# Optimization experiments

Hardware: AMD Instinct MI355X
Metric: run time of the kernel (lower is better)

The kernel has to match this reference:

```python
import jax, jax.numpy as jnp
import numpy as np
from jax import lax

EPS = 1e-5

def _layernorm(x, g, b):
    m = jnp.mean(x, axis=-1, keepdims=True)
    v = jnp.mean((x - m) ** 2, axis=-1, keepdims=True)
    return (x - m) * lax.rsqrt(v + EPS) * g + b

def _dwconv(x, H, W, w, b):
    # x: [B, N, C], w: [C, 1, 3, 3] (OIHW, depthwise), b: [C]
    B, N, C = x.shape
    xi = x.transpose(0, 2, 1).reshape(B, C, H, W)
    y = lax.conv_general_dilated(
        xi, w, window_strides=(1, 1), padding='SAME',
        feature_group_count=C,
        dimension_numbers=('NCHW', 'OIHW', 'NCHW'))
    y = y + b[None, :, None, None]
    return y.reshape(B, C, H * W).transpose(0, 2, 1)

def _channel_attn(x, groups, qkv_w, qkv_b, proj_w, proj_b):
    B, N, C = x.shape
    hd = C // groups
    qkv = x @ qkv_w.T + qkv_b                       # [B, N, 3C]
    qkv = qkv.reshape(B, N, 3, groups, hd)
    q, k, v = qkv[:, :, 0], qkv[:, :, 1], qkv[:, :, 2]   # [B, N, g, hd]
    q = q * (float(N) ** -0.5)
    attn = jnp.einsum('bngc,bngd->bgcd', q, k)      # [B, g, hd, hd]
    attn = jax.nn.softmax(attn, axis=-1)
    out = jnp.einsum('bgcd,bngd->bngc', attn, v)    # [B, N, g, hd]
    out = out.reshape(B, N, C)
    return out @ proj_w.T + proj_b

def _block(x, H, W, dw1_w, dw1_b, ln1_g, ln1_b, qkv_w, qkv_b, proj_w, proj_b,
           dw2_w, dw2_b, ln2_g, ln2_b, fc1_w, fc1_b, fc2_w, fc2_b, groups=8):
    # conv1 (no norm) + residual
    x = x + _dwconv(x, H, W, dw1_w, dw1_b)
    # prenorm channel attention + residual
    x = x + _channel_attn(_layernorm(x, ln1_g, ln1_b), groups, qkv_w, qkv_b, proj_w, proj_b)
    # conv2 (no norm) + residual
    x = x + _dwconv(x, H, W, dw2_w, dw2_b)
    # prenorm MLP + residual
    h = _layernorm(x, ln2_g, ln2_b)
    h = jax.nn.gelu(h @ fc1_w.T + fc1_b, approximate=False)
    x = x + (h @ fc2_w.T + fc2_b)
    return x

def setup_inputs() -> dict:
    key = jax.random.key(0)
    B, H, W, C, groups, ratio = 32, 32, 32, 768, 8, 4
    N, Ch = H * W, C * ratio
    ks = jax.random.split(key, 16)
    s = lambda fan: 1.0 / np.sqrt(fan)
    return {
        'x': jax.random.normal(ks[0], (B, N, C), jnp.float32),
        'H': H, 'W': W,
        'dw1_w': jax.random.normal(ks[1], (C, 1, 3, 3), jnp.float32) * s(9),
        'dw1_b': jnp.zeros((C,), jnp.float32),
        'ln1_g': jnp.ones((C,), jnp.float32),
        'ln1_b': jnp.zeros((C,), jnp.float32),
        'qkv_w': jax.random.normal(ks[2], (3 * C, C), jnp.float32) * s(C),
        'qkv_b': jnp.zeros((3 * C,), jnp.float32),
        'proj_w': jax.random.normal(ks[3], (C, C), jnp.float32) * s(C),
        'proj_b': jnp.zeros((C,), jnp.float32),
        'dw2_w': jax.random.normal(ks[4], (C, 1, 3, 3), jnp.float32) * s(9),
        'dw2_b': jnp.zeros((C,), jnp.float32),
        'ln2_g': jnp.ones((C,), jnp.float32),
        'ln2_b': jnp.zeros((C,), jnp.float32),
        'fc1_w': jax.random.normal(ks[5], (Ch, C), jnp.float32) * s(C),
        'fc1_b': jnp.zeros((Ch,), jnp.float32),
        'fc2_w': jax.random.normal(ks[6], (C, Ch), jnp.float32) * s(Ch),
        'fc2_b': jnp.zeros((C,), jnp.float32),
    }

def reference(x, H, W, dw1_w, dw1_b, ln1_g, ln1_b, qkv_w, qkv_b, proj_w, proj_b,
              dw2_w, dw2_b, ln2_g, ln2_b, fc1_w, fc1_b, fc2_w, fc2_b):
    return _block(x, H, W, dw1_w, dw1_b, ln1_g, ln1_b, qkv_w, qkv_b, proj_w, proj_b,
                  dw2_w, dw2_b, ln2_g, ln2_b, fc1_w, fc1_b, fc2_w, fc2_b)
```

## Files before the change

kernel.cpp:

```cpp
#include <hip/hip_runtime.h>

typedef unsigned short ushort_t;
typedef __bf16 v8bf __attribute__((ext_vector_type(8)));
typedef float v4f __attribute__((ext_vector_type(4)));

#define B_ 32
#define N_ 1024
#define C_ 768
#define G_ 8
#define HD_ 96
#define CH_ 3072
#define M_ 32768

static __device__ __forceinline__ float b2f(ushort_t u) {
    union { float f; unsigned int i; } z; z.i = ((unsigned int)u) << 16; return z.f;
}
static __device__ __forceinline__ ushort_t f2b(float f) {
    unsigned int u = __float_as_uint(f);
    u += 0x7fff + ((u >> 16) & 1);
    return (ushort_t)(u >> 16);
}
static __device__ __forceinline__ unsigned int pk2(float a, float b) {
    return (unsigned int)f2b(a) | ((unsigned int)f2b(b) << 16);
}

#define GLOAD_LDS16(g, l) __builtin_amdgcn_global_load_lds( \
    (const __attribute__((address_space(1))) unsigned int*)(g), \
    (__attribute__((address_space(3))) unsigned int*)(l), 16, 0, 0)

__global__ __launch_bounds__(256) void cvt_all(
    const float* __restrict__ a, const float* __restrict__ b,
    const float* __restrict__ c, const float* __restrict__ d,
    ushort_t* __restrict__ o)
{
    int blk = blockIdx.x;
    const float* src; ushort_t* dst; int off;
    if (blk < 1728)      { src = a; dst = o;                          off = blk; }
    else if (blk < 2304) { src = b; dst = o + 2304 * 768;             off = blk - 1728; }
    else if (blk < 4608) { src = c; dst = o + 2304 * 768 + 768 * 768; off = blk - 2304; }
    else                 { src = d; dst = o + 2304 * 768 + 768 * 768 + 3072 * 768; off = blk - 4608; }
    int i = (off * 256 + threadIdx.x) * 4;
    float4 v = *(const float4*)(src + i);
    uint2 p; p.x = pk2(v.x, v.y); p.y = pk2(v.z, v.w);
    *(uint2*)(dst + i) = p;
}

__global__ __launch_bounds__(256) void transpose_w2(
    const float* __restrict__ w1, const float* __restrict__ w2,
    float* __restrict__ wt1, float* __restrict__ wt2)
{
    int blk = blockIdx.x;
    const float* w = (blk < 27) ? w1 : w2;
    float* wt = (blk < 27) ? wt1 : wt2;
    int i = (blk % 27) * 256 + threadIdx.x;
    int c = i / 9, k = i % 9;
    wt[k * C_ + c] = w[i];
}

__global__ __launch_bounds__(256) void dwconv_add(
    const float* __restrict__ xin, const float* __restrict__ wt,
    const float* __restrict__ bias, float* __restrict__ out)
{
    int t = threadIdx.x;
    int bid = blockIdx.x;
    int cblk = bid % 6;
    int bhp = bid / 6;
    int b = bhp >> 4, hp = bhp & 15;
    int h0 = hp * 2;
    int tw = t >> 5;
    int c0 = cblk * 128 + (t & 31) * 4;
    int w0 = tw * 4;

    float4 tap[4][6];
#pragma unroll
    for (int dh = 0; dh < 4; dh++) {
        int hh = h0 + dh - 1;
        bool hok = (hh >= 0) && (hh < 32);
#pragma unroll
        for (int dw = 0; dw < 6; dw++) {
            int ww = w0 + dw - 1;
            bool ok = hok && (ww >= 0) && (ww < 32);
            if (ok)
                tap[dh][dw] = *(const float4*)(
                    xin + (size_t)((b << 10) | (hh << 5) | ww) * C_ + c0);
            else
                tap[dh][dw] = make_float4(0.f, 0.f, 0.f, 0.f);
        }
    }
    float4 wv[9];
#pragma unroll
    for (int k = 0; k < 9; k++)
        wv[k] = *(const float4*)(wt + k * C_ + c0);
    float4 bv = *(const float4*)(bias + c0);

#pragma unroll
    for (int row = 0; row < 2; row++) {
#pragma unroll
        for (int i = 0; i < 4; i++) {
            float4 acc = bv;
#pragma unroll
            for (int dh = 0; dh < 3; dh++)
#pragma unroll
                for (int dw = 0; dw < 3; dw++) {
                    float4 xv = tap[row + dh][i + dw];
                    float4 wk = wv[dh * 3 + dw];
                    acc.x += wk.x * xv.x; acc.y += wk.y * xv.y;
                    acc.z += wk.z * xv.z; acc.w += wk.w * xv.w;
                }
            float4 xr = tap[row + 1][i + 1];
            acc.x += xr.x; acc.y += xr.y; acc.z += xr.z; acc.w += xr.w;
            *(float4*)(out + (size_t)((b << 10) | ((h0 + row) << 5) | (w0 + i)) * C_ + c0) = acc;
        }
    }
}

__global__ __launch_bounds__(256) void layernorm_bf(
    const float* __restrict__ xin, const float* __restrict__ g,
    const float* __restrict__ bb, ushort_t* __restrict__ out)
{
    int row = blockIdx.x;
    int t = threadIdx.x;
    const float* xr = xin + (size_t)row * C_;
    float x0 = xr[t], x1 = xr[t + 256], x2 = xr[t + 512];
    float s1 = x0 + x1 + x2;
    float s2 = x0 * x0 + x1 * x1 + x2 * x2;
#pragma unroll
    for (int o = 32; o > 0; o >>= 1) {
        s1 += __shfl_xor(s1, o);
        s2 += __shfl_xor(s2, o);
    }
    __shared__ float red[8];
    if ((t & 63) == 0) { red[(t >> 6) * 2] = s1; red[(t >> 6) * 2 + 1] = s2; }
    __syncthreads();
    s1 = red[0] + red[2] + red[4] + red[6];
    s2 = red[1] + red[3] + red[5] + red[7];
    float m = s1 * (1.0f / 768.0f);
    float var = s2 * (1.0f / 768.0f) - m * m;
    float inv = rsqrtf(var + 1e-5f);
    ushort_t* orow = out + (size_t)row * C_;
    orow[t]       = f2b((x0 - m) * inv * g[t]       + bb[t]);
    orow[t + 256] = f2b((x1 - m) * inv * g[t + 256] + bb[t + 256]);
    orow[t + 512] = f2b((x2 - m) * inv * g[t + 512] + bb[t + 512]);
}

template <int EPI>
__global__ __launch_bounds__(256) void gemm_bt(
    const ushort_t* __restrict__ A, const ushort_t* __restrict__ W,
    const float* __restrict__ bias, const float* __restrict__ resid,
    void* __restrict__ outv, int M, int Nf, int K)
{
    __shared__ __align__(16) ushort_t ring[3][2][128 * 32];
    int t = threadIdx.x;
    int bm = blockIdx.x;
    int bn = blockIdx.y;
    int wave = t >> 6, lane = t & 63;
    int wm = (wave >> 1) * 64;
    int wn = (wave & 1) * 64;
    int row16 = lane & 15;
    int quad = lane >> 4;
    int qswz = (quad * 8) ^ (((row16 >> 1) & 3) * 8);

    int r0 = wave * 16 + (lane >> 2);
    int r1 = (wave + 4) * 16 + (lane >> 2);
    int c8s = ((lane & 3) ^ ((lane >> 3) & 3)) * 8;
    const ushort_t* Ag0 = A + (size_t)(bm * 128 + r0) * K + c8s;
    const ushort_t* Ag1 = A + (size_t)(bm * 128 + r1) * K + c8s;
    const ushort_t* Wg0 = W + (size_t)(bn * 128 + r0) * K + c8s;
    const ushort_t* Wg1 = W + (size_t)(bn * 128 + r1) * K + c8s;

    v4f acc[4][4];
#pragma unroll
    for (int i = 0; i < 4; i++)
#pragma unroll
        for (int j = 0; j < 4; j++) acc[i][j] = (v4f){0.f, 0.f, 0.f, 0.f};

    const int NT = K >> 5;

    auto STAGE = [&](int kt) {
        int s = kt % 3;
        ushort_t* a = &ring[s][0][0];
        ushort_t* b = &ring[s][1][0];
        int off = kt * 32;
        GLOAD_LDS16(Ag0 + off, a + wave * 512);
        GLOAD_LDS16(Ag1 + off, a + (wave + 4) * 512);
        GLOAD_LDS16(Wg0 + off, b + wave * 512);
        GLOAD_LDS16(Wg1 + off, b + (wave + 4) * 512);
    };

    STAGE(0);
    STAGE(1);
    asm volatile("s_waitcnt vmcnt(4)" ::: "memory");
    __builtin_amdgcn_s_barrier();

    for (int kt = 0; kt < NT; ++kt) {
        if (kt + 2 < NT) STAGE(kt + 2);

        const ushort_t* sA = &ring[kt % 3][0][0];
        const ushort_t* sB = &ring[kt % 3][1][0];
        v8bf af[4], bfr[4];
#pragma unroll
        for (int i = 0; i < 4; i++)
            af[i] = *(const v8bf*)(sA + (wm + i * 16 + row16) * 32 + qswz);
#pragma unroll
        for (int j = 0; j < 4; j++)
            bfr[j] = *(const v8bf*)(sB + (wn + j * 16 + row16) * 32 + qswz);
#pragma unroll
        for (int i = 0; i < 4; i++)
#pragma unroll
            for (int j = 0; j < 4; j++)
                acc[i][j] = __builtin_amdgcn_mfma_f32_16x16x32_bf16(af[i], bfr[j], acc[i][j], 0, 0, 0);

        if (kt + 1 < NT) {
            if (kt + 2 < NT)
                asm volatile("s_waitcnt vmcnt(4)" ::: "memory");
            else
                asm volatile("s_waitcnt vmcnt(0)" ::: "memory");
            __builtin_amdgcn_s_barrier();
        }
    }

#pragma unroll
    for (int i = 0; i < 4; i++) {
#pragma unroll
        for (int j = 0; j < 4; j++) {
            int col = bn * 128 + wn + j * 16 + row16;
            float bv = bias[col];
#pragma unroll
            for (int r = 0; r < 4; r++) {
                int row = bm * 128 + wm + i * 16 + quad * 4 + r;
                float v = acc[i][j][r] + bv;
                if (EPI == 1) v = 0.5f * v * (1.0f + erff(v * 0.70710678118f));
                if (EPI == 2) {
                    v += resid[(size_t)row * Nf + col];
                    ((float*)outv)[(size_t)row * Nf + col] = v;
                } else {
                    ((ushort_t*)outv)[(size_t)row * Nf + col] = f2b(v);
                }
            }
        }
    }
}

__global__ __launch_bounds__(256) void chan_attn(
    const ushort_t* __restrict__ qkv, ushort_t* __restrict__ P)
{
    __shared__ __align__(16) char smem[96 * 97 * 4];
    ushort_t* sQt = (ushort_t*)smem;
    ushort_t* sKt = (ushort_t*)(smem + 13824);
    float* sS = (float*)smem;
    int bg = blockIdx.x;
    int b = bg >> 3, g = bg & 7;
    int t = threadIdx.x;
    int wave = t >> 6, lane = t & 63;
    int wc = (wave >> 1) * 48, wd = (wave & 1) * 48;
    int row16 = lane & 15, quad = lane >> 4;

    int li0 = t * 3;
    int r_[3], sg_[3];
#pragma unroll
    for (int i = 0; i < 3; i++) { r_[i] = (li0 + i) / 12; sg_[i] = (li0 + i) % 12; }

    v4f acc[3][3];
#pragma unroll
    for (int i = 0; i < 3; i++)
#pragma unroll
        for (int j = 0; j < 3; j++) acc[i][j] = (v4f){0.f, 0.f, 0.f, 0.f};

    uint4 uq[3], uk[3];
#pragma unroll
    for (int i = 0; i < 3; i++) {
        const ushort_t* p = qkv + ((size_t)(b * N_ + r_[i]) * 3) * C_ + g * HD_ + sg_[i] * 8;
        uq[i] = *(const uint4*)p;
        uk[i] = *(const uint4*)(p + C_);
    }

    for (int n0 = 0; n0 < N_; n0 += 64) {
        uint4 nq[3] = {}, nk[3] = {};
        bool more = (n0 + 64 < N_);
        if (more) {
#pragma unroll
            for (int i = 0; i < 3; i++) {
                const ushort_t* p = qkv + ((size_t)(b * N_ + n0 + 64 + r_[i]) * 3) * C_ + g * HD_ + sg_[i] * 8;
                nq[i] = *(const uint4*)p;
                nk[i] = *(const uint4*)(p + C_);
            }
        }
        __syncthreads();
#pragma unroll
        for (int i = 0; i < 3; i++) {
            union { uint4 v; ushort_t s[8]; } a, bu;
            a.v = uq[i]; bu.v = uk[i];
#pragma unroll
            for (int k2 = 0; k2 < 8; k2++) {
                sQt[(sg_[i] * 8 + k2) * 72 + r_[i]] = a.s[k2];
                sKt[(sg_[i] * 8 + k2) * 72 + r_[i]] = bu.s[k2];
            }
        }
        __syncthreads();
#pragma unroll
        for (int kk = 0; kk < 64; kk += 32) {
            v8bf af[3], bf2[3];
#pragma unroll
            for (int i = 0; i < 3; i++)
                af[i] = *(const v8bf*)(sQt + (wc + i * 16 + row16) * 72 + kk + quad * 8);
#pragma unroll
            for (int j = 0; j < 3; j++)
                bf2[j] = *(const v8bf*)(sKt + (wd + j * 16 + row16) * 72 + kk + quad * 8);
#pragma unroll
            for (int i = 0; i < 3; i++)
#pragma unroll
                for (int j = 0; j < 3; j++)
                    acc[i][j] = __builtin_amdgcn_mfma_f32_16x16x32_bf16(af[i], bf2[j], acc[i][j], 0, 0, 0);
        }
        if (more) {
#pragma unroll
            for (int i = 0; i < 3; i++) { uq[i] = nq[i]; uk[i] = nk[i]; }
        }
    }
    __syncthreads();
#pragma unroll
    for (int i = 0; i < 3; i++)
#pragma unroll
        for (int j = 0; j < 3; j++)
#pragma unroll
            for (int r = 0; r < 4; r++) {
                int c = wc + i * 16 + quad * 4 + r;
                int d = wd + j * 16 + row16;
                sS[c * 97 + d] = acc[i][j][r] * 0.03125f;
            }
    __syncthreads();
    if (t < 96) {
        float mx = -1e30f;
        for (int d = 0; d < 96; d++) mx = fmaxf(mx, sS[t * 97 + d]);
        float sum = 0.f;
        for (int d = 0; d < 96; d++) sum += __expf(sS[t * 97 + d] - mx);
        float rs = 1.0f / sum;
        ushort_t* prow = P + (size_t)bg * 9216 + t * 96;
        for (int d = 0; d < 96; d++) prow[d] = f2b(__expf(sS[t * 97 + d] - mx) * rs);
    }
}

__global__ __launch_bounds__(256) void attn_av(
    const ushort_t* __restrict__ qkv, const ushort_t* __restrict__ P,
    ushort_t* __restrict__ out)
{
    __shared__ __align__(16) ushort_t sV[256 * 104];
    __shared__ __align__(16) ushort_t sP[96 * 104];
    int blk = blockIdx.x;
    int nch = blk & 3, g = (blk >> 2) & 7, b = blk >> 5;
    int t = threadIdx.x;
    int n0 = nch * 256;
#pragma unroll
    for (int i = 0; i < 12; i++) {
        int li = t + i * 256;
        int r = li / 12, sg = li % 12;
        size_t voff = ((size_t)(b * N_ + n0 + r) * 3 + 2) * C_ + g * HD_ + sg * 8;
        *(uint4*)(sV + r * 104 + sg * 8) = *(const uint4*)(qkv + voff);
    }
#pragma unroll
    for (int i = 0; i < 5; i++) {
        int li = t + i * 256;
        if (li < 1152) {
            int r = li / 12, sg = li % 12;
            *(uint4*)(sP + r * 104 + sg * 8) =
                *(const uint4*)(P + (size_t)(b * 8 + g) * 9216 + li * 8);
        }
    }
    __syncthreads();
    int wave = t >> 6, lane = t & 63;
    int wm = wave * 64;
    int row16 = lane & 15, quad = lane >> 4;
    v4f acc[4][6];
#pragma unroll
    for (int i = 0; i < 4; i++)
#pragma unroll
        for (int j = 0; j < 6; j++) acc[i][j] = (v4f){0.f, 0.f, 0.f, 0.f};
#pragma unroll
    for (int kk = 0; kk < 96; kk += 32) {
        v8bf af[4], bfr[6];
#pragma unroll
        for (int i = 0; i < 4; i++)
            af[i] = *(const v8bf*)(sV + (wm + i * 16 + row16) * 104 + kk + quad * 8);
#pragma unroll
        for (int j = 0; j < 6; j++)
            bfr[j] = *(const v8bf*)(sP + (j * 16 + row16) * 104 + kk + quad * 8);
#pragma unroll
        for (int i = 0; i < 4; i++)
#pragma unroll
            for (int j = 0; j < 6; j++)
                acc[i][j] = __builtin_amdgcn_mfma_f32_16x16x32_bf16(af[i], bfr[j], acc[i][j], 0, 0, 0);
    }
#pragma unroll
    for (int i = 0; i < 4; i++)
#pragma unroll
        for (int j = 0; j < 6; j++)
#pragma unroll
            for (int r = 0; r < 4; r++) {
                int n = n0 + wm + i * 16 + quad * 4 + r;
                int c = j * 16 + row16;
                out[(size_t)(b * N_ + n) * C_ + g * HD_ + c] = f2b(acc[i][j][r]);
            }
}

extern "C" void kernel_launch(void* const* d_in, const int* in_sizes, int n_in,
                              void* d_out, int out_size, void* d_ws, size_t ws_size,
                              hipStream_t stream)
{
    const float* x      = (const float*)d_in[0];
    const float* dw1_w  = (const float*)d_in[3];
    const float* dw1_b  = (const float*)d_in[4];
    const float* ln1_g  = (const float*)d_in[5];
    const float* ln1_b  = (const float*)d_in[6];
    const float* qkv_w  = (const float*)d_in[7];
    const float* qkv_b  = (const float*)d_in[8];
    const float* proj_w = (const float*)d_in[9];
    const float* proj_b = (const float*)d_in[10];
    const float* dw2_w  = (const float*)d_in[11];
    const float* dw2_b  = (const float*)d_in[12];
    const float* ln2_g  = (const float*)d_in[13];
    const float* ln2_b  = (const float*)d_in[14];
    const float* fc1_w  = (const float*)d_in[15];
    const float* fc1_b  = (const float*)d_in[16];
    const float* fc2_w  = (const float*)d_in[17];
    const float* fc2_b  = (const float*)d_in[18];
    float* outp = (float*)d_out;

    char* ws = (char*)d_ws;
    ushort_t* qkvW = (ushort_t*)ws;
    ushort_t* projW = qkvW + 2304 * 768;
    ushort_t* fc1W = projW + 768 * 768;
    ushort_t* fc2W = fc1W + 3072 * 768;
    const size_t WB = (size_t)(2304*768 + 768*768 + 3072*768 + 768*3072) * 2;
    float* wt1 = (float*)(ws + WB);
    float* wt2 = wt1 + 9 * C_;
    const size_t WTB = 2 * 9 * C_ * sizeof(float);

    size_t CB = 32;
    while (CB > 1 && WB + WTB + CB * 12730368ull > ws_size) CB >>= 1;
    const size_t R = CB * 1024;
    char* act = ws + WB + WTB;
    ushort_t* L  = (ushort_t*)act;
    ushort_t* Ab = (ushort_t*)(act + R * C_ * 2);
    float*    X2 = (float*)(act + 2 * R * C_ * 2);
    ushort_t* P  = (ushort_t*)(act + 2 * R * C_ * 2 + R * C_ * 4);
    ushort_t* D  = (ushort_t*)(act + 2 * R * C_ * 2 + R * C_ * 4 + CB * 147456);

    cvt_all<<<6912, 256, 0, stream>>>(qkv_w, proj_w, fc1_w, fc2_w, qkvW);
    transpose_w2<<<54, 256, 0, stream>>>(dw1_w, dw2_w, wt1, wt2);

    dwconv_add<<<32 * 16 * 6, 256, 0, stream>>>(x, wt1, dw1_b, outp);

    const int nchunk = (int)(32 / CB);
    for (int c = 0; c < nchunk; c++) {
        float* xc = outp + (size_t)c * R * C_;
        layernorm_bf<<<(int)R, 256, 0, stream>>>(xc, ln1_g, ln1_b, L);
        gemm_bt<0><<<dim3((int)R / 128, 2304 / 128), 256, 0, stream>>>(
            L, qkvW, qkv_b, nullptr, D, (int)R, 2304, C_);
        chan_attn<<<(int)CB * 8, 256, 0, stream>>>(D, P);
        attn_av<<<(int)CB * 32, 256, 0, stream>>>(D, P, Ab);
        gemm_bt<2><<<dim3((int)R / 128, C_ / 128), 256, 0, stream>>>(
            Ab, projW, proj_b, xc, X2, (int)R, C_, C_);
        dwconv_add<<<(int)(R / 1024) * 16 * 6, 256, 0, stream>>>(X2, wt2, dw2_b, xc);
        layernorm_bf<<<(int)R, 256, 0, stream>>>(xc, ln2_g, ln2_b, L);
        gemm_bt<1><<<dim3((int)R / 128, CH_ / 128), 256, 0, stream>>>(
            L, fc1W, fc1_b, nullptr, D, (int)R, CH_, C_);
        gemm_bt<2><<<dim3((int)R / 128, C_ / 128), 256, 0, stream>>>(
            D, fc2W, fc2_b, xc, xc, (int)R, C_, CH_);
    }
}
```

Before: 1.153 ms.

## Unroll GEMM main loop by ring depth, add MFMA priority, use tanh-GELU

Unrolls the triple-buffered GEMM K loop by three, so ring-stage indices and LDS pointers are precomputed constants instead of computed with kt%3 each iteration. Raises wave priority around the MFMA block and hoists bias loads in the epilogue. It also replaces the exact erf-based GELU with the tanh approximation written via exp, which cuts epilogue math but departs from the reference's exact GELU. The unrolled loop assumes K is a multiple of 96.

```diff
diff --git a/kernel.cpp b/kernel.cpp
--- a/kernel.cpp
+++ b/kernel.cpp
@@ -149,7 +149,7 @@
     const float* __restrict__ bias, const float* __restrict__ resid,
     void* __restrict__ outv, int M, int Nf, int K)
 {
-    __shared__ __align__(16) ushort_t ring[3][2][128 * 32];
+    __shared__ __align__(16) ushort_t ring[3][2][4096];
     int t = threadIdx.x;
     int bm = blockIdx.x;
     int bn = blockIdx.y;
@@ -168,73 +168,93 @@
     const ushort_t* Wg0 = W + (size_t)(bn * 128 + r0) * K + c8s;
     const ushort_t* Wg1 = W + (size_t)(bn * 128 + r1) * K + c8s;
 
+    ushort_t *stA0[3], *stA1[3], *stB0[3], *stB1[3];
+    const ushort_t *rdA[3], *rdB[3];
+#pragma unroll
+    for (int s = 0; s < 3; s++) {
+        stA0[s] = &ring[s][0][0] + wave * 512;
+        stA1[s] = &ring[s][0][0] + (wave + 4) * 512;
+        stB0[s] = &ring[s][1][0] + wave * 512;
+        stB1[s] = &ring[s][1][0] + (wave + 4) * 512;
+        rdA[s]  = &ring[s][0][0] + (wm + row16) * 32 + qswz;
+        rdB[s]  = &ring[s][1][0] + (wn + row16) * 32 + qswz;
+    }
+
     v4f acc[4][4];
 #pragma unroll
     for (int i = 0; i < 4; i++)
 #pragma unroll
         for (int j = 0; j < 4; j++) acc[i][j] = (v4f){0.f, 0.f, 0.f, 0.f};
 
-    const int NT = K >> 5;
-
-    auto STAGE = [&](int kt) {
-        int s = kt % 3;
-        ushort_t* a = &ring[s][0][0];
-        ushort_t* b = &ring[s][1][0];
-        int off = kt * 32;
-        GLOAD_LDS16(Ag0 + off, a + wave * 512);
-        GLOAD_LDS16(Ag1 + off, a + (wave + 4) * 512);
-        GLOAD_LDS16(Wg0 + off, b + wave * 512);
-        GLOAD_LDS16(Wg1 + off, b + (wave + 4) * 512);
+    auto STAGE = [&](int s, int off) {
+        GLOAD_LDS16(Ag0 + off, stA0[s]);
+        GLOAD_LDS16(Ag1 + off, stA1[s]);
+        GLOAD_LDS16(Wg0 + off, stB0[s]);
+        GLOAD_LDS16(Wg1 + off, stB1[s]);
     };
-
-    STAGE(0);
-    STAGE(1);
+    auto COMPUTE = [&](int s) {
+        v8bf af[4], bfr[4];
+#pragma unroll
+        for (int i = 0; i < 4; i++) af[i] = *(const v8bf*)(rdA[s] + i * 512);
+#pragma unroll
+        for (int j = 0; j < 4; j++) bfr[j] = *(const v8bf*)(rdB[s] + j * 512);
+        __builtin_amdgcn_s_setprio(1);
+#pragma unroll
+        for (int i = 0; i < 4; i++)
+#pragma unroll
+            for (int j = 0; j < 4; j++)
+                acc[i][j] = __builtin_amdgcn_mfma_f32_16x16x32_bf16(af[i], bfr[j], acc[i][j], 0, 0, 0);
+        __builtin_amdgcn_s_setprio(0);
+    };
+
+    STAGE(0, 0);
+    STAGE(1, 32);
     asm volatile("s_waitcnt vmcnt(4)" ::: "memory");
     __builtin_amdgcn_s_barrier();
 
-    for (int kt = 0; kt < NT; ++kt) {
-        if (kt + 2 < NT) STAGE(kt + 2);
-
-        const ushort_t* sA = &ring[kt % 3][0][0];
-        const ushort_t* sB = &ring[kt % 3][1][0];
-        v8bf af[4], bfr[4];
-#pragma unroll
-        for (int i = 0; i < 4; i++)
-            af[i] = *(const v8bf*)(sA + (wm + i * 16 + row16) * 32 + qswz);
-#pragma unroll
-        for (int j = 0; j < 4; j++)
-            bfr[j] = *(const v8bf*)(sB + (wn + j * 16 + row16) * 32 + qswz);
-#pragma unroll
-        for (int i = 0; i < 4; i++)
-#pragma unroll
-            for (int j = 0; j < 4; j++)
-                acc[i][j] = __builtin_amdgcn_mfma_f32_16x16x32_bf16(af[i], bfr[j], acc[i][j], 0, 0, 0);
-
-        if (kt + 1 < NT) {
-            if (kt + 2 < NT)
-                asm volatile("s_waitcnt vmcnt(4)" ::: "memory");
-            else
-                asm volatile("s_waitcnt vmcnt(0)" ::: "memory");
-            __builtin_amdgcn_s_barrier();
-        }
-    }
-
+    const int NG = K / 96;
+    for (int g = 0; g < NG - 1; ++g) {
+        STAGE(2, 64);  COMPUTE(0);
+        asm volatile("s_waitcnt vmcnt(4)" ::: "memory");
+        __builtin_amdgcn_s_barrier();
+        STAGE(0, 96);  COMPUTE(1);
+        asm volatile("s_waitcnt vmcnt(4)" ::: "memory");
+        __builtin_amdgcn_s_barrier();
+        STAGE(1, 128); COMPUTE(2);
+        asm volatile("s_waitcnt vmcnt(4)" ::: "memory");
+        __builtin_amdgcn_s_barrier();
+        Ag0 += 96; Ag1 += 96; Wg0 += 96; Wg1 += 96;
+    }
+    STAGE(2, 64); COMPUTE(0);
+    asm volatile("s_waitcnt vmcnt(4)" ::: "memory");
+    __builtin_amdgcn_s_barrier();
+    COMPUTE(1);
+    asm volatile("s_waitcnt vmcnt(0)" ::: "memory");
+    __builtin_amdgcn_s_barrier();
+    COMPUTE(2);
+
+    float bv[4];
+#pragma unroll
+    for (int j = 0; j < 4; j++) bv[j] = bias[bn * 128 + wn + j * 16 + row16];
+    int col0 = bn * 128 + wn + row16;
 #pragma unroll
     for (int i = 0; i < 4; i++) {
-#pragma unroll
-        for (int j = 0; j < 4; j++) {
-            int col = bn * 128 + wn + j * 16 + row16;
-            float bv = bias[col];
-#pragma unroll
-            for (int r = 0; r < 4; r++) {
-                int row = bm * 128 + wm + i * 16 + quad * 4 + r;
-                float v = acc[i][j][r] + bv;
-                if (EPI == 1) v = 0.5f * v * (1.0f + erff(v * 0.70710678118f));
+        int rowb = bm * 128 + wm + i * 16 + quad * 4;
+#pragma unroll
+        for (int r = 0; r < 4; r++) {
+            size_t rb = (size_t)(rowb + r) * Nf + col0;
+#pragma unroll
+            for (int j = 0; j < 4; j++) {
+                float v = acc[i][j][r] + bv[j];
+                if (EPI == 1) {
+                    float u = v * (0.7978845608f + 0.0356774081f * v * v);
+                    v = v / (1.0f + __expf(-2.0f * u));
+                }
                 if (EPI == 2) {
-                    v += resid[(size_t)row * Nf + col];
-                    ((float*)outv)[(size_t)row * Nf + col] = v;
+                    v += resid[rb + j * 16];
+                    ((float*)outv)[rb + j * 16] = v;
                 } else {
-                    ((ushort_t*)outv)[(size_t)row * Nf + col] = f2b(v);
+                    ((ushort_t*)outv)[rb + j * 16] = f2b(v);
                 }
             }
         }
```

Measured after the change: 1.099 ms. -4.7%, faster.
